# Optimization experiments

Measured on AMD Instinct MI355X. Metric: run time of the kernel, lower is better.

The kernel has to match this reference:

```python
import jax, jax.numpy as jnp
import numpy as np

EMBED = 1024

def setup_inputs() -> dict:
    key = jax.random.key(0)
    kx, kq, kk, kv = jax.random.split(key, 4)
    x = jax.random.normal(kx, (4, 2048, EMBED), dtype=jnp.float32)
    s = 1.0 / np.sqrt(EMBED)
    Wq = jax.random.normal(kq, (EMBED, EMBED), dtype=jnp.float32) * s
    Wk = jax.random.normal(kk, (EMBED, EMBED), dtype=jnp.float32) * s
    Wv = jax.random.normal(kv, (EMBED, EMBED), dtype=jnp.float32) * s
    return {"x": x, "Wq": Wq, "Wk": Wk, "Wv": Wv}

def reference(x, Wq, Wk, Wv):
    # x: [b, s, e]; nn.Linear(y) = y @ W.T, weights stored [out, in]
    Q = jnp.einsum('bse,oe->bso', x, Wq)
    K = jnp.einsum('bse,oe->bso', x, Wk)
    V = jnp.einsum('bse,oe->bso', x, Wv)
    scale = 1.0 / jnp.sqrt(jnp.asarray(x.shape[-1], x.dtype))
    energy = jnp.einsum('bqe,bke->bqk', Q, K) * scale  # [b, s, s]
    attention = jax.nn.softmax(energy, axis=-1)
    out = jnp.einsum('bqk,bke->bqe', attention, V)
    return out
```

## Files before the change

### kernel.cpp

```cpp
#include <hip/hip_runtime.h>
#include <stdint.h>


typedef __attribute__((ext_vector_type(8))) short bf16x8;
typedef __attribute__((ext_vector_type(4))) float f32x4;

__device__ __forceinline__ float bf2f(uint16_t u) {
    return __uint_as_float(((uint32_t)u) << 16);
}
__device__ __forceinline__ uint16_t f2bf(float f) {
    uint32_t u = __float_as_uint(f);
    uint32_t r = u + 0x7FFFu + ((u >> 16) & 1u);
    return (uint16_t)(r >> 16);
}

__device__ __forceinline__ void gll16(const void* g, void* l) {
    __builtin_amdgcn_global_load_lds(
        (const __attribute__((address_space(1))) uint32_t*)g,
        (__attribute__((address_space(3))) uint32_t*)l,
        16, 0, 0);
}

__global__ __launch_bounds__(256) void cast_all(const float* __restrict__ x,
                                                const float* __restrict__ Wq,
                                                const float* __restrict__ Wk,
                                                const float* __restrict__ Wv,
                                                uint16_t* __restrict__ xb,
                                                uint16_t* __restrict__ wqkvb,
                                                int NX4, int NW4) {
    int i = blockIdx.x * 256 + threadIdx.x;
    const float* src;
    uint16_t* dst;
    int off;
    if (i < NX4) {
        src = x; dst = xb; off = i;
    } else {
        int j = i - NX4;
        if (j >= 3 * NW4) return;
        int which = j / NW4;
        off = j - which * NW4;
        src = (which == 0) ? Wq : (which == 1) ? Wk : Wv;
        dst = wqkvb + (size_t)which * NW4 * 4;
    }
    float4 v = ((const float4*)src)[off];
    ushort4 o;
    o.x = f2bf(v.x); o.y = f2bf(v.y); o.z = f2bf(v.z); o.w = f2bf(v.w);
    ((ushort4*)dst)[off] = o;
}

__global__ __launch_bounds__(256) void softmax_rows(uint16_t* __restrict__ P) {
    const int n = 2048;
    uint16_t* row = P + (size_t)blockIdx.x * n;
    int tid = threadIdx.x;
    int w = tid >> 6, ln = tid & 63;
    float v[8];
    float m = -3.4e38f;
    #pragma unroll
    for (int i = 0; i < 8; i++) { v[i] = bf2f(row[tid + 256 * i]); m = fmaxf(m, v[i]); }
    #pragma unroll
    for (int o = 32; o >= 1; o >>= 1) m = fmaxf(m, __shfl_down(m, o, 64));
    __shared__ float smax[4], ssum[4];
    if (ln == 0) smax[w] = m;
    __syncthreads();
    m = fmaxf(fmaxf(smax[0], smax[1]), fmaxf(smax[2], smax[3]));
    float s = 0.f;
    #pragma unroll
    for (int i = 0; i < 8; i++) { v[i] = __expf(v[i] - m); s += v[i]; }
    #pragma unroll
    for (int o = 32; o >= 1; o >>= 1) s += __shfl_down(s, o, 64);
    if (ln == 0) ssum[w] = s;
    __syncthreads();
    s = ssum[0] + ssum[1] + ssum[2] + ssum[3];
    float inv = 1.f / s;
    #pragma unroll
    for (int i = 0; i < 8; i++) row[tid + 256 * i] = f2bf(v[i] * inv);
}


#define DS_A(mh_) do { \
    _Pragma("unroll") for (int f_ = 0; f_ < MH; ++f_) { \
        const uint16_t* p_ = Asb + axbase + ((mh_)*MH + f_) * 1024; \
        af[f_][0] = *(const bf16x8*)(p_ + cs0); \
        af[f_][1] = *(const bf16x8*)(p_ + cs1); \
    } } while (0)

#define DS_B(nh_) do { \
    _Pragma("unroll") for (int n_ = 0; n_ < 2; ++n_) { \
        const uint16_t* p_ = Bsb + bxbase + ((nh_)*2 + n_) * 1024; \
        bfr[nh_][n_][0] = *(const bf16x8*)(p_ + cs0); \
        bfr[nh_][n_][1] = *(const bf16x8*)(p_ + cs1); \
    } } while (0)

#define MMA(mh_, nh_) do { \
    _Pragma("unroll") for (int f_ = 0; f_ < MH; ++f_) { \
        _Pragma("unroll") for (int n_ = 0; n_ < 2; ++n_) { \
            acc[(mh_)*MH + f_][(nh_)*2 + n_] = __builtin_amdgcn_mfma_f32_16x16x32_bf16( \
                af[f_][0], bfr[nh_][n_][0], acc[(mh_)*MH + f_][(nh_)*2 + n_], 0, 0, 0); \
            acc[(mh_)*MH + f_][(nh_)*2 + n_] = __builtin_amdgcn_mfma_f32_16x16x32_bf16( \
                af[f_][1], bfr[nh_][n_][1], acc[(mh_)*MH + f_][(nh_)*2 + n_], 0, 0, 0); \
        } } } while (0)

#define PH_ENTER do { \
    asm volatile("s_barrier\n\ts_waitcnt lgkmcnt(0)" ::: "memory"); \
    __builtin_amdgcn_s_setprio(1); } while (0)

#define PH_EXIT do { \
    __builtin_amdgcn_s_setprio(0); \
    asm volatile("s_barrier" ::: "memory"); } while (0)

#define VMB(n) asm volatile("s_waitcnt vmcnt(" #n ")\n\ts_barrier" ::: "memory")
#define BARO   asm volatile("s_barrier" ::: "memory")
#define NOBAR  ((void)0)

#define KTILE(ISSUE, W1B, W3B) do { \
    const uint16_t* Asb = &As[cur][0]; \
    const uint16_t* Bsb = &Bs[cur][0]; \
     \
    DS_A(0); DS_B(0); \
    PH_ENTER; MMA(0, 0); PH_EXIT; \
     \
    DS_B(1); \
    if constexpr (BM == 256) { if (ISSUE) { stA(cur, ko2, 0); stA(cur, ko2, 2); } } \
    PH_ENTER; MMA(0, 1); __builtin_amdgcn_s_setprio(0); W1B; \
     \
    DS_A(1); \
    if (ISSUE) { stB(cur, ko2, 0); stB(cur, ko2, 1); stB(cur, ko2, 2); stB(cur, ko2, 3); } \
    PH_ENTER; MMA(1, 0); PH_EXIT; \
     \
    if (ISSUE) { \
        if constexpr (BM == 256) { stA(cur, ko2, 1); stA(cur, ko2, 3); } \
        else                     { stA(cur, ko2, 0); stA(cur, ko2, 1); } \
    } \
    PH_ENTER; MMA(1, 1); __builtin_amdgcn_s_setprio(0); W3B; \
} while (0)

template <int BM, typename OutT>
__global__ __launch_bounds__(512, 2) void gemm_nt(const uint16_t* __restrict__ A,
                                                  const uint16_t* __restrict__ B,
                                                  OutT* __restrict__ C,
                                                  int gx, int gy,
                                                  long lda, long ldb, long ldc,
                                                  int K, float alpha,
                                                  long sA, long sB, long sC,
                                                  uint16_t* __restrict__ VtP,
                                                  int vcol0) {
    constexpr int MF = BM / 32;
    constexpr int MH = MF / 2;

    const int total = gridDim.x;
    const int nb  = blockIdx.x;
    const int per = total >> 3;
    const int g   = (nb & 7) * per + (nb >> 3);
    const int pb  = gx * gy;
    const int bz  = g / pb;
    const int r   = g - bz * pb;
    const int stpr = gx >> 2;
    const int st  = r >> 4;
    const int w   = r & 15;
    const int sty = st / stpr;
    const int stx = st - sty * stpr;
    const int bx  = (stx << 2) + (w & 3);
    const int by  = (sty << 2) + (w >> 2);

    A += (long)bz * sA;
    B += (long)bz * sB;
    C += (long)bz * sC;

    __shared__ uint16_t As[2][BM * 64];
    __shared__ uint16_t Bs[2][256 * 64];

    const int tid = threadIdx.x;
    const int m0 = by * BM;
    const int n0 = bx * 256;

    const int srow = tid >> 3;
    const int sx   = ((tid & 7) ^ (srow & 7)) << 3;
    const uint16_t* Ag = A + (long)(m0 + srow) * lda + sx;
    const uint16_t* Bg = B + (long)(n0 + srow) * ldb + sx;

    auto stA = [&](int buf, long ko, int c) {
        gll16(Ag + (long)c * 64 * lda + ko, &As[buf][c * 4096] + tid * 8);
    };
    auto stB = [&](int buf, long ko, int c) {
        gll16(Bg + (long)c * 64 * ldb + ko, &Bs[buf][c * 4096] + tid * 8);
    };

    const int wave = tid >> 6, lane = tid & 63;
    const int quad = lane >> 4, l16 = lane & 15;
    const int wm = wave >> 2, wn = wave & 3;
    const int cs0 = ((quad       ^ (l16 & 7)) << 3);
    const int cs1 = (((quad + 4) ^ (l16 & 7)) << 3);
    const int axbase = (wm * (BM / 2) + l16) * 64;
    const int bxbase = (wn * 64 + l16) * 64;

    const int nk = K / 64;

    f32x4 acc[MF][4] = {};
    bf16x8 af[MH][2];
    bf16x8 bfr[2][2][2];

    if constexpr (BM == 256) {
        stA(0, 0, 0);  stA(0, 0, 2);
        stB(0, 0, 0);  stB(0, 0, 1);  stB(0, 0, 2);  stB(0, 0, 3);
        stA(0, 0, 1);  stA(0, 0, 3);
        stA(1, 64, 0); stA(1, 64, 2);
        stB(1, 64, 0); stB(1, 64, 1); stB(1, 64, 2); stB(1, 64, 3);
        stA(1, 64, 1); stA(1, 64, 3);
        VMB(10);
    } else {
        stB(0, 0, 0);  stB(0, 0, 1);  stB(0, 0, 2);  stB(0, 0, 3);
        stA(0, 0, 0);  stA(0, 0, 1);
        stB(1, 64, 0); stB(1, 64, 1); stB(1, 64, 2); stB(1, 64, 3);
        stA(1, 64, 0); stA(1, 64, 1);
        VMB(6);
    }

    int cur = 0;
    for (int kt = 0; kt < nk - 2; ++kt) {
        const long ko2 = (long)(kt + 2) * 64;
        if constexpr (BM == 256) { KTILE(1, VMB(10), VMB(10)); }
        else                     { KTILE(1, BARO,    VMB(6));  }
        cur ^= 1;
    }
    {
        const long ko2 = 0; (void)ko2;
        if constexpr (BM == 256) { KTILE(0, VMB(8), VMB(2)); }
        else                     { KTILE(0, BARO,   VMB(0)); }
        cur ^= 1;
    }
    {
        const long ko2 = 0; (void)ko2;
        if constexpr (BM == 256) { KTILE(0, VMB(0), NOBAR); }
        else                     { KTILE(0, BARO,   NOBAR); }
    }

    if (VtP && n0 >= vcol0) {
        #pragma unroll
        for (int f = 0; f < MF; ++f) {
            const int row0 = m0 + wm * (BM / 2) + f * 16 + quad * 4;
            const int b_   = row0 >> 11;
            const int s_   = row0 & 2047;
            #pragma unroll
            for (int j = 0; j < 4; ++j) {
                const int e = n0 + wn * 64 + j * 16 + l16 - vcol0;
                ushort4 o;
                o.x = f2bf(acc[f][j][0]);
                o.y = f2bf(acc[f][j][1]);
                o.z = f2bf(acc[f][j][2]);
                o.w = f2bf(acc[f][j][3]);
                *(ushort4*)(VtP + ((long)b_ * 1024 + e) * 2048 + s_) = o;
            }
        }
    } else {
        #pragma unroll
        for (int f = 0; f < MF; ++f) {
            #pragma unroll
            for (int j = 0; j < 4; ++j) {
                #pragma unroll
                for (int r4 = 0; r4 < 4; ++r4) {
                    const int row = m0 + wm * (BM / 2) + f * 16 + quad * 4 + r4;
                    const int col = n0 + wn * 64 + j * 16 + l16;
                    const float val = acc[f][j][r4] * alpha;
                    if constexpr (sizeof(OutT) == 2)
                        C[(long)row * ldc + col] = f2bf(val);
                    else
                        C[(long)row * ldc + col] = val;
                }
            }
        }
    }
}

extern "C" void kernel_launch(void* const* d_in, const int* in_sizes, int n_in,
                              void* d_out, int out_size, void* d_ws, size_t ws_size,
                              hipStream_t stream) {
    const float* x  = (const float*)d_in[0];
    const float* Wq = (const float*)d_in[1];
    const float* Wk = (const float*)d_in[2];
    const float* Wv = (const float*)d_in[3];
    float* out = (float*)d_out;

    const int Bn = 4, S = 2048, E = 1024;
    const long MS = (long)Bn * S;
    const int  N3 = 3 * E;

    char* ws = (char*)d_ws;
    uint16_t* xb    = (uint16_t*)ws;  ws += (size_t)MS * E * 2;
    uint16_t* wqkvb = (uint16_t*)ws;  ws += (size_t)N3 * E * 2;
    uint16_t* QKb   = (uint16_t*)ws;  ws += (size_t)MS * 2048 * 2;
    uint16_t* Vt    = (uint16_t*)ws;  ws += (size_t)Bn * E * S * 2;
    uint16_t* Pb    = (uint16_t*)ws;  ws += (size_t)Bn * S * S * 2;

    {
        int NX4 = (int)(MS * E / 4);
        int NW4 = E * E / 4;
        int tot = NX4 + 3 * NW4;
        cast_all<<<dim3((tot + 255) / 256), dim3(256), 0, stream>>>(
            x, Wq, Wk, Wv, xb, wqkvb, NX4, NW4);
    }

    {
        int gx = N3 / 256, gy = (int)(MS / 128);
        gemm_nt<128, uint16_t><<<dim3(gx * gy), dim3(512), 0, stream>>>(
            xb, wqkvb, QKb, gx, gy, E, E, 2048, E, 1.f, 0, 0, 0,
            Vt, 2048);
    }

    {
        int gx = S / 256, gy = S / 256;
        gemm_nt<256, uint16_t><<<dim3(gx * gy * Bn), dim3(512), 0, stream>>>(
            QKb, QKb + 1024, Pb, gx, gy, 2048, 2048, S, E, 0.03125f,
            (long)S * 2048, (long)S * 2048, (long)S * S,
            nullptr, 0);
    }

    softmax_rows<<<dim3(Bn * S), dim3(256), 0, stream>>>(Pb);

    {
        int gx = E / 256, gy = S / 128;
        gemm_nt<128, float><<<dim3(gx * gy * Bn), dim3(512), 0, stream>>>(
            Pb, Vt, out, gx, gy, S, S, E, S, 1.f,
            (long)S * S, (long)E * S, (long)S * E,
            nullptr, 0);
    }
}
```

Before: 252.8 us.

## Prefetch next-tile LDS fragments across phases and drop BM=256 GEMM variant

Restructures the GEMM k-loop so the first A/B fragments of the next k-tile are read from the other LDS buffer during the last MFMA phase, overlapping LDS reads with compute. Each phase now has explicit sched_barriers and priority toggles, and there are fewer waitcnt points. The kernel is specialised to a single 128x256 tile, so the QK^T GEMM now uses 128-row tiles with twice as many blocks. This trades some operand reuse per block for more parallelism and simpler scheduling, and it uses more registers for the double-buffered fragments.

```diff
diff --git a/kernel.cpp b/kernel.cpp
--- a/kernel.cpp
+++ b/kernel.cpp
@@ -77,64 +77,67 @@
 }
 
 
-#define DS_A(mh_) do { \
-    _Pragma("unroll") for (int f_ = 0; f_ < MH; ++f_) { \
-        const uint16_t* p_ = Asb + axbase + ((mh_)*MH + f_) * 1024; \
-        af[f_][0] = *(const bf16x8*)(p_ + cs0); \
-        af[f_][1] = *(const bf16x8*)(p_ + cs1); \
-    } } while (0)
-
-#define DS_B(nh_) do { \
+#define DS_A0(P_) do { _Pragma("unroll") for (int f_ = 0; f_ < 2; ++f_) { \
+    const uint16_t* q_ = (P_) + axbase + f_ * 1024; \
+    a0[f_][0] = *(const bf16x8*)(q_ + cs0); \
+    a0[f_][1] = *(const bf16x8*)(q_ + cs1); } } while (0)
+
+#define DS_A1(P_) do { _Pragma("unroll") for (int f_ = 0; f_ < 2; ++f_) { \
+    const uint16_t* q_ = (P_) + axbase + (2 + f_) * 1024; \
+    a1[f_][0] = *(const bf16x8*)(q_ + cs0); \
+    a1[f_][1] = *(const bf16x8*)(q_ + cs1); } } while (0)
+
+#define DS_B0(P_) do { _Pragma("unroll") for (int n_ = 0; n_ < 2; ++n_) { \
+    const uint16_t* q_ = (P_) + bxbase + n_ * 1024; \
+    b0[n_][0] = *(const bf16x8*)(q_ + cs0); \
+    b0[n_][1] = *(const bf16x8*)(q_ + cs1); } } while (0)
+
+#define DS_B1(P_) do { _Pragma("unroll") for (int n_ = 0; n_ < 2; ++n_) { \
+    const uint16_t* q_ = (P_) + bxbase + (2 + n_) * 1024; \
+    b1[n_][0] = *(const bf16x8*)(q_ + cs0); \
+    b1[n_][1] = *(const bf16x8*)(q_ + cs1); } } while (0)
+
+#define MMA_(AF_, BF_, I_, J_) do { \
+    _Pragma("unroll") for (int f_ = 0; f_ < 2; ++f_) \
     _Pragma("unroll") for (int n_ = 0; n_ < 2; ++n_) { \
-        const uint16_t* p_ = Bsb + bxbase + ((nh_)*2 + n_) * 1024; \
-        bfr[nh_][n_][0] = *(const bf16x8*)(p_ + cs0); \
-        bfr[nh_][n_][1] = *(const bf16x8*)(p_ + cs1); \
-    } } while (0)
-
-#define MMA(mh_, nh_) do { \
-    _Pragma("unroll") for (int f_ = 0; f_ < MH; ++f_) { \
-        _Pragma("unroll") for (int n_ = 0; n_ < 2; ++n_) { \
-            acc[(mh_)*MH + f_][(nh_)*2 + n_] = __builtin_amdgcn_mfma_f32_16x16x32_bf16( \
-                af[f_][0], bfr[nh_][n_][0], acc[(mh_)*MH + f_][(nh_)*2 + n_], 0, 0, 0); \
-            acc[(mh_)*MH + f_][(nh_)*2 + n_] = __builtin_amdgcn_mfma_f32_16x16x32_bf16( \
-                af[f_][1], bfr[nh_][n_][1], acc[(mh_)*MH + f_][(nh_)*2 + n_], 0, 0, 0); \
-        } } } while (0)
-
-#define PH_ENTER do { \
-    asm volatile("s_barrier\n\ts_waitcnt lgkmcnt(0)" ::: "memory"); \
-    __builtin_amdgcn_s_setprio(1); } while (0)
-
-#define PH_EXIT do { \
-    __builtin_amdgcn_s_setprio(0); \
-    asm volatile("s_barrier" ::: "memory"); } while (0)
-
+        acc[(I_) + f_][(J_) + n_] = __builtin_amdgcn_mfma_f32_16x16x32_bf16( \
+            AF_[f_][0], BF_[n_][0], acc[(I_) + f_][(J_) + n_], 0, 0, 0); \
+        acc[(I_) + f_][(J_) + n_] = __builtin_amdgcn_mfma_f32_16x16x32_bf16( \
+            AF_[f_][1], BF_[n_][1], acc[(I_) + f_][(J_) + n_], 0, 0, 0); } } while (0)
+
+#define MMA00 MMA_(a0, b0, 0, 0)
+#define MMA01 MMA_(a0, b1, 0, 2)
+#define MMA10 MMA_(a1, b0, 2, 0)
+#define MMA11 MMA_(a1, b1, 2, 2)
+
+#define PRIO1 __builtin_amdgcn_s_setprio(1)
+#define PRIO0 __builtin_amdgcn_s_setprio(0)
+#define BAR   asm volatile("s_barrier" ::: "memory")
+#define SB0   __builtin_amdgcn_sched_barrier(0)
 #define VMB(n) asm volatile("s_waitcnt vmcnt(" #n ")\n\ts_barrier" ::: "memory")
-#define BARO   asm volatile("s_barrier" ::: "memory")
-#define NOBAR  ((void)0)
-
-#define KTILE(ISSUE, W1B, W3B) do { \
-    const uint16_t* Asb = &As[cur][0]; \
-    const uint16_t* Bsb = &Bs[cur][0]; \
-     \
-    DS_A(0); DS_B(0); \
-    PH_ENTER; MMA(0, 0); PH_EXIT; \
-     \
-    DS_B(1); \
-    if constexpr (BM == 256) { if (ISSUE) { stA(cur, ko2, 0); stA(cur, ko2, 2); } } \
-    PH_ENTER; MMA(0, 1); __builtin_amdgcn_s_setprio(0); W1B; \
-     \
-    DS_A(1); \
-    if (ISSUE) { stB(cur, ko2, 0); stB(cur, ko2, 1); stB(cur, ko2, 2); stB(cur, ko2, 3); } \
-    PH_ENTER; MMA(1, 0); PH_EXIT; \
-     \
-    if (ISSUE) { \
-        if constexpr (BM == 256) { stA(cur, ko2, 1); stA(cur, ko2, 3); } \
-        else                     { stA(cur, ko2, 0); stA(cur, ko2, 1); } \
-    } \
-    PH_ENTER; MMA(1, 1); __builtin_amdgcn_s_setprio(0); W3B; \
+
+#define KTILE(G, R3, WT) do { \
+    const uint16_t* Asb  = &As[cur][0]; \
+    const uint16_t* Bsb  = &Bs[cur][0]; \
+    const uint16_t* AsbN = &As[cur ^ 1][0]; \
+    const uint16_t* BsbN = &Bs[cur ^ 1][0]; \
+     \
+    DS_B1(Bsb); \
+    BAR; SB0; PRIO1; MMA00; PRIO0; SB0; BAR; \
+     \
+    DS_A1(Asb); \
+    BAR; SB0; PRIO1; MMA01; PRIO0; SB0; BAR; \
+     \
+    if (G) { stB(cur, ko2, 0); stB(cur, ko2, 1); stB(cur, ko2, 2); stB(cur, ko2, 3); } \
+    BAR; SB0; PRIO1; MMA10; PRIO0; SB0; WT; \
+     \
+     \
+    if (R3) { DS_A0(AsbN); DS_B0(BsbN); } \
+    if (G) { stA(cur, ko2, 0); stA(cur, ko2, 1); } \
+    BAR; SB0; PRIO1; MMA11; PRIO0; SB0; BAR; \
 } while (0)
 
-template <int BM, typename OutT>
+template <typename OutT>
 __global__ __launch_bounds__(512, 2) void gemm_nt(const uint16_t* __restrict__ A,
                                                   const uint16_t* __restrict__ B,
                                                   OutT* __restrict__ C,
@@ -144,9 +147,6 @@
                                                   long sA, long sB, long sC,
                                                   uint16_t* __restrict__ VtP,
                                                   int vcol0) {
-    constexpr int MF = BM / 32;
-    constexpr int MH = MF / 2;
-
     const int total = gridDim.x;
     const int nb  = blockIdx.x;
     const int per = total >> 3;
@@ -166,11 +166,11 @@
     B += (long)bz * sB;
     C += (long)bz * sC;
 
-    __shared__ uint16_t As[2][BM * 64];
+    __shared__ uint16_t As[2][128 * 64];
     __shared__ uint16_t Bs[2][256 * 64];
 
     const int tid = threadIdx.x;
-    const int m0 = by * BM;
+    const int m0 = by * 128;
     const int n0 = bx * 256;
 
     const int srow = tid >> 3;
@@ -190,54 +190,44 @@
     const int wm = wave >> 2, wn = wave & 3;
     const int cs0 = ((quad       ^ (l16 & 7)) << 3);
     const int cs1 = (((quad + 4) ^ (l16 & 7)) << 3);
-    const int axbase = (wm * (BM / 2) + l16) * 64;
+    const int axbase = (wm * 64 + l16) * 64;
     const int bxbase = (wn * 64 + l16) * 64;
 
     const int nk = K / 64;
 
-    f32x4 acc[MF][4] = {};
-    bf16x8 af[MH][2];
-    bf16x8 bfr[2][2][2];
-
-    if constexpr (BM == 256) {
-        stA(0, 0, 0);  stA(0, 0, 2);
-        stB(0, 0, 0);  stB(0, 0, 1);  stB(0, 0, 2);  stB(0, 0, 3);
-        stA(0, 0, 1);  stA(0, 0, 3);
-        stA(1, 64, 0); stA(1, 64, 2);
-        stB(1, 64, 0); stB(1, 64, 1); stB(1, 64, 2); stB(1, 64, 3);
-        stA(1, 64, 1); stA(1, 64, 3);
-        VMB(10);
-    } else {
-        stB(0, 0, 0);  stB(0, 0, 1);  stB(0, 0, 2);  stB(0, 0, 3);
-        stA(0, 0, 0);  stA(0, 0, 1);
-        stB(1, 64, 0); stB(1, 64, 1); stB(1, 64, 2); stB(1, 64, 3);
-        stA(1, 64, 0); stA(1, 64, 1);
-        VMB(6);
-    }
+    f32x4 acc[4][4] = {};
+    bf16x8 a0[2][2], a1[2][2];
+    bf16x8 b0[2][2], b1[2][2];
+
+    stB(0, 0, 0);  stB(0, 0, 1);  stB(0, 0, 2);  stB(0, 0, 3);
+    stA(0, 0, 0);  stA(0, 0, 1);
+    stB(1, 64, 0); stB(1, 64, 1); stB(1, 64, 2); stB(1, 64, 3);
+    stA(1, 64, 0); stA(1, 64, 1);
+    asm volatile("s_waitcnt vmcnt(6)" ::: "memory");
+    BAR;
+    { const uint16_t* P = &As[0][0]; DS_A0(P); }
+    { const uint16_t* Q = &Bs[0][0]; DS_B0(Q); }
 
     int cur = 0;
     for (int kt = 0; kt < nk - 2; ++kt) {
         const long ko2 = (long)(kt + 2) * 64;
-        if constexpr (BM == 256) { KTILE(1, VMB(10), VMB(10)); }
-        else                     { KTILE(1, BARO,    VMB(6));  }
+        KTILE(1, 1, VMB(4));
         cur ^= 1;
     }
     {
         const long ko2 = 0; (void)ko2;
-        if constexpr (BM == 256) { KTILE(0, VMB(8), VMB(2)); }
-        else                     { KTILE(0, BARO,   VMB(0)); }
+        KTILE(0, 1, VMB(0));
         cur ^= 1;
     }
     {
         const long ko2 = 0; (void)ko2;
-        if constexpr (BM == 256) { KTILE(0, VMB(0), NOBAR); }
-        else                     { KTILE(0, BARO,   NOBAR); }
+        KTILE(0, 0, BAR);
     }
 
     if (VtP && n0 >= vcol0) {
         #pragma unroll
-        for (int f = 0; f < MF; ++f) {
-            const int row0 = m0 + wm * (BM / 2) + f * 16 + quad * 4;
+        for (int f = 0; f < 4; ++f) {
+            const int row0 = m0 + wm * 64 + f * 16 + quad * 4;
             const int b_   = row0 >> 11;
             const int s_   = row0 & 2047;
             #pragma unroll
@@ -253,12 +243,12 @@
         }
     } else {
         #pragma unroll
-        for (int f = 0; f < MF; ++f) {
+        for (int f = 0; f < 4; ++f) {
             #pragma unroll
             for (int j = 0; j < 4; ++j) {
                 #pragma unroll
                 for (int r4 = 0; r4 < 4; ++r4) {
-                    const int row = m0 + wm * (BM / 2) + f * 16 + quad * 4 + r4;
+                    const int row = m0 + wm * 64 + f * 16 + quad * 4 + r4;
                     const int col = n0 + wn * 64 + j * 16 + l16;
                     const float val = acc[f][j][r4] * alpha;
                     if constexpr (sizeof(OutT) == 2)
@@ -301,14 +291,14 @@
 
     {
         int gx = N3 / 256, gy = (int)(MS / 128);
-        gemm_nt<128, uint16_t><<<dim3(gx * gy), dim3(512), 0, stream>>>(
+        gemm_nt<uint16_t><<<dim3(gx * gy), dim3(512), 0, stream>>>(
             xb, wqkvb, QKb, gx, gy, E, E, 2048, E, 1.f, 0, 0, 0,
             Vt, 2048);
     }
 
     {
-        int gx = S / 256, gy = S / 256;
-        gemm_nt<256, uint16_t><<<dim3(gx * gy * Bn), dim3(512), 0, stream>>>(
+        int gx = S / 256, gy = S / 128;
+        gemm_nt<uint16_t><<<dim3(gx * gy * Bn), dim3(512), 0, stream>>>(
             QKb, QKb + 1024, Pb, gx, gy, 2048, 2048, S, E, 0.03125f,
             (long)S * 2048, (long)S * 2048, (long)S * S,
             nullptr, 0);
@@ -318,7 +308,7 @@
 
     {
         int gx = E / 256, gy = S / 128;
-        gemm_nt<128, float><<<dim3(gx * gy * Bn), dim3(512), 0, stream>>>(
+        gemm_nt<float><<<dim3(gx * gy * Bn), dim3(512), 0, stream>>>(
             Pb, Vt, out, gx, gy, S, S, E, S, 1.f,
             (long)S * S, (long)E * S, (long)S * E,
             nullptr, 0);
```

Result: slower. 277.5 us (+9.8%).
